# Kernel tuning notes

Measured on AMD Instinct MI355X. Metric: run time of the kernel, lower is better.

Reference implementation:

```python
import jax, jax.numpy as jnp
import numpy as np

N_WIDTH = 16
N_ORDER = 3
N_ELEMENTS = 64
N_NODES = N_ELEMENTS * N_ORDER + 1  # 193
N_SAMPLES = 4096
X_MIN = 0.0
X_MAX = 1.0
NDIM_IN = 2


def setup_inputs() -> dict:
    key = jax.random.key(0)
    k1, k2 = jax.random.split(key)
    x = jax.random.uniform(k1, (N_SAMPLES, NDIM_IN), dtype=jnp.float32)  # in [x_min, x_max]
    # torch init is zeros; use small random values so outputs/grads are informative
    weight = 0.1 * jax.random.normal(k2, (N_WIDTH, N_NODES, NDIM_IN), dtype=jnp.float32)
    return {"x": x, "weight": weight}


def _lagrange_all(xr, nodes):
    """phi, dphi, ddphi of the (n_order+1) Lagrange basis at xr (S,W,D).
    Returns three arrays of shape (S,W,P,D), P = n_order+1. Loops are over the
    tiny fixed basis size only; everything is vectorized over (S,W,D)."""
    P = len(nodes)
    phi, dphi, ddphi = [], [], []
    for j in range(P):
        # value
        p = jnp.ones_like(xr)
        for m in range(P):
            if m != j:
                p = p * (xr - nodes[m]) / (nodes[j] - nodes[m])
        phi.append(p)
        # first derivative
        y1 = jnp.zeros_like(xr)
        for i in range(P):
            if i == j:
                continue
            k = jnp.full_like(xr, 1.0 / (nodes[j] - nodes[i]))
            for m in range(P):
                if m != i and m != j:
                    k = k * (xr - nodes[m]) / (nodes[j] - nodes[m])
            y1 = y1 + k
        dphi.append(y1)
        # second derivative
        y2 = jnp.zeros_like(xr)
        for i in range(P):
            if i == j:
                continue
            ks = jnp.zeros_like(xr)
            for m in range(P):
                if m != i and m != j:
                    kp = jnp.full_like(xr, 1.0 / (nodes[j] - nodes[m]))
                    for n in range(P):
                        if n != i and n != j and n != m:
                            kp = kp * (xr - nodes[n]) / (nodes[j] - nodes[n])
                    ks = ks + kp
            y2 = y2 + ks / (nodes[j] - nodes[i])
        ddphi.append(y2)
    return jnp.stack(phi, 2), jnp.stack(dphi, 2), jnp.stack(ddphi, 2)


def _forward(x, weight):
    S, W, D, P = N_SAMPLES, N_WIDTH, NDIM_IN, N_ORDER + 1
    xw = jnp.broadcast_to(x[:, None, :], (S, W, D))  # (S,W,D)
    x_shift = (N_NODES - 1) * (xw - X_MIN) / (X_MAX - X_MIN)
    id_el = jnp.clip(jnp.floor(x_shift / N_ORDER), 0, N_ELEMENTS - 1)
    nodes_l = (id_el * N_ORDER).astype(jnp.int32)  # (S,W,D), left node index
    # nodes_r - nodes_l == n_order
    x_ref = 2.0 * (x_shift - nodes_l) / N_ORDER - 1.0
    delta_x = 0.5 * N_ORDER * (X_MAX - X_MIN) / (N_NODES - 1)

    nodes = [float(v) for v in np.linspace(-1.0, 1.0, P)]
    phi_l, dphi_l, ddphi_l = _lagrange_all(x_ref, nodes)  # (S,W,P,D)
    dphi_l = dphi_l / delta_x
    ddphi_l = ddphi_l / (delta_x * delta_x)

    # Scatter local basis values into global node axis (vectorized replacement
    # of the quadruple Python loop in the original).
    ii = jnp.arange(S)[:, None, None, None]
    kk = jnp.arange(W)[None, :, None, None]
    dd = jnp.arange(D)[None, None, None, :]
    pp = nodes_l[:, :, None, :] + jnp.arange(P)[None, None, :, None]  # (S,W,P,D)
    zeros = jnp.zeros((S, W, N_NODES, D), dtype=x.dtype)
    phi = zeros.at[ii, kk, pp, dd].set(phi_l)
    dphi = zeros.at[ii, kk, pp, dd].set(dphi_l)
    ddphi = zeros.at[ii, kk, pp, dd].set(ddphi_l)

    t_ik = jnp.einsum('kpj,ikpj->ik', weight, phi)
    dt_ik = jnp.einsum('kpj,ikpj->ik', weight, dphi)
    ddt_ik = jnp.einsum('kpj,ikpj->ik', weight, ddphi)
    return t_ik, dt_ik, ddt_ik, phi, dphi, ddphi, delta_x


def reference(x, weight):
    # returns (t_ik, dt_ik, ddt_ik, phi_ikpj, dphi_ikpj, ddphi_ikpj, delta_x)
    return _forward(x, weight)
```

## Files before the change

### kernel.cpp

```cpp
#include <hip/hip_runtime.h>

constexpr int S  = 4096;
constexpr int W  = 16;
constexpr int NN = 193;
constexpr int DD = 2;
constexpr int SW = S * W;
constexpr int PHI_OFF = 3 * SW;
constexpr int PHI_SZ  = SW * NN * DD;
constexpr int DX_OFF  = PHI_OFF + 3 * PHI_SZ;

constexpr int ROW_F  = NN * DD;
constexpr int ROW_F2 = NN;
constexpr int CHUNK_F2 = W * ROW_F2;

__global__ __launch_bounds__(256)
void kan_fused_kernel(const float* __restrict__ x,
                      const float* __restrict__ w,
                      float* __restrict__ out) {
    const int i   = blockIdx.x;
    const int tid = threadIdx.x;

    __shared__ __align__(16) float row[3][ROW_F];
    __shared__ float vals[3][DD][4];
    __shared__ int   nls[DD];

    for (int idx = tid; idx < 3 * ROW_F; idx += 256)
        (&row[0][0])[idx] = 0.0f;

    if (tid < DD) {
        const int d = tid;
        float xv = x[i * DD + d];
        float xs = 192.0f * xv;
        float fe = floorf(xs / 3.0f);
        fe = fminf(fmaxf(fe, 0.0f), 63.0f);
        int nl = (int)(fe * 3.0f);
        nls[d] = nl;
        float xr = 2.0f * (xs - (float)nl) / 3.0f - 1.0f;

        float xp1 = xr + 1.0f;
        float xm1 = xr - 1.0f;
        float x2  = xr * xr;
        float x2m = x2 - (1.0f / 9.0f);
        const float c0 = 0.5625f;
        const float c1 = 1.6875f;

        vals[0][d][0] = -c0 * x2m * xm1;
        vals[0][d][1] =  c1 * xp1 * (xr - (1.0f / 3.0f)) * xm1;
        vals[0][d][2] = -c1 * xp1 * (xr + (1.0f / 3.0f)) * xm1;
        vals[0][d][3] =  c0 * xp1 * x2m;

        const float idx1 = 128.0f;
        vals[1][d][0] = -c0 * (3.0f * x2 - 2.0f * xr - (1.0f / 9.0f)) * idx1;
        vals[1][d][1] =  c1 * (3.0f * x2 - (2.0f / 3.0f) * xr - 1.0f) * idx1;
        vals[1][d][2] = -c1 * (3.0f * x2 + (2.0f / 3.0f) * xr - 1.0f) * idx1;
        vals[1][d][3] =  c0 * (3.0f * x2 + 2.0f * xr - (1.0f / 9.0f)) * idx1;

        const float idx2 = 16384.0f;
        vals[2][d][0] = -c0 * (6.0f * xr - 2.0f) * idx2;
        vals[2][d][1] =  c1 * (6.0f * xr - (2.0f / 3.0f)) * idx2;
        vals[2][d][2] = -c1 * (6.0f * xr + (2.0f / 3.0f)) * idx2;
        vals[2][d][3] =  c0 * (6.0f * xr + 2.0f) * idx2;
    }

    __syncthreads();

    if (tid < 24) {
        int a = tid >> 3;
        int r = tid & 7;
        int d = r >> 2;
        int p = r & 3;
        row[a][(nls[d] + p) * DD + d] = vals[a][d][p];
    }

    if (tid < 48) {
        int k = tid / 3;
        int a = tid % 3;
        float s = 0.0f;
#pragma unroll
        for (int d = 0; d < DD; ++d) {
            int base = k * (NN * DD) + nls[d] * DD + d;
#pragma unroll
            for (int p = 0; p < 4; ++p)
                s += w[base + p * DD] * vals[a][d][p];
        }
        out[a * SW + i * W + k] = s;
    }

    if (i == 0 && tid == 0)
        out[DX_OFF] = 0.0078125f;

    __syncthreads();

#pragma unroll
    for (int a = 0; a < 3; ++a) {
        float2* dst = (float2*)(out + PHI_OFF + a * PHI_SZ) + (size_t)i * CHUNK_F2;
        const float2* src = (const float2*)(&row[a][0]);
        for (int idx = tid; idx < CHUNK_F2; idx += 256) {
            int j = idx % ROW_F2;
            dst[idx] = src[j];
        }
    }
}

extern "C" void kernel_launch(void* const* d_in, const int* in_sizes, int n_in,
                              void* d_out, int out_size, void* d_ws, size_t ws_size,
                              hipStream_t stream) {
    const float* x = (const float*)d_in[0];
    const float* w = (const float*)d_in[1];
    float* out = (float*)d_out;

    kan_fused_kernel<<<S, 256, 0, stream>>>(x, w, out);
}
```

Measured before the change: 302.6 us.

## Process eight samples per block with 16-byte nontemporal stores of phi rows

Each block now handles 8 samples instead of 1 and builds padded shared-memory rows for all of them. The phi, dphi and ddphi output is written as 16-byte vectors with nontemporal stores instead of 8-byte float2 stores. Row wrap-around is handled by padding each row so a 4-float read can cross the row end. This is meant to raise store width and cut per-block overhead on a kernel limited by output writes, at the cost of fewer blocks and more shared memory per block.

```diff
diff --git a/kernel.cpp b/kernel.cpp
--- a/kernel.cpp
+++ b/kernel.cpp
@@ -9,32 +9,44 @@
 constexpr int PHI_SZ  = SW * NN * DD;
 constexpr int DX_OFF  = PHI_OFF + 3 * PHI_SZ;
 
-constexpr int ROW_F  = NN * DD;
-constexpr int ROW_F2 = NN;
-constexpr int CHUNK_F2 = W * ROW_F2;
+constexpr int ROW_F   = NN * DD;
+constexpr int ROW_PAD = 392;
+constexpr int R       = 8;
+constexpr int NB      = S / R;
+constexpr int CHUNK_F = W * ROW_F;
+constexpr int BLK_F4  = R * CHUNK_F / 4;
+constexpr int FULL_IT = BLK_F4 / 256;
+constexpr int TAIL    = BLK_F4 - FULL_IT * 256;
+constexpr int STEP_J  = 1024 % ROW_F;
+
+typedef float f32x4 __attribute__((ext_vector_type(4)));
 
 __global__ __launch_bounds__(256)
 void kan_fused_kernel(const float* __restrict__ x,
                       const float* __restrict__ w,
                       float* __restrict__ out) {
-    const int i   = blockIdx.x;
+    const int bx  = blockIdx.x;
     const int tid = threadIdx.x;
 
-    __shared__ __align__(16) float row[3][ROW_F];
-    __shared__ float vals[3][DD][4];
-    __shared__ int   nls[DD];
+    __shared__ __align__(16) float row[3][R][ROW_PAD];
+    __shared__ float vals[3][R][DD][4];
+    __shared__ int   nls[R][DD];
 
-    for (int idx = tid; idx < 3 * ROW_F; idx += 256)
-        (&row[0][0])[idx] = 0.0f;
+    {
+        f32x4* rz = (f32x4*)&row[0][0][0];
+        for (int idx = tid; idx < 3 * R * ROW_PAD / 4; idx += 256)
+            rz[idx] = (f32x4){0.f, 0.f, 0.f, 0.f};
+    }
 
-    if (tid < DD) {
-        const int d = tid;
-        float xv = x[i * DD + d];
+    if (tid < R * DD) {
+        const int smp = tid >> 1;
+        const int d   = tid & 1;
+        float xv = x[(bx * R + smp) * DD + d];
         float xs = 192.0f * xv;
         float fe = floorf(xs / 3.0f);
         fe = fminf(fmaxf(fe, 0.0f), 63.0f);
         int nl = (int)(fe * 3.0f);
-        nls[d] = nl;
+        nls[smp][d] = nl;
         float xr = 2.0f * (xs - (float)nl) / 3.0f - 1.0f;
 
         float xp1 = xr + 1.0f;
@@ -44,60 +56,92 @@
         const float c0 = 0.5625f;
         const float c1 = 1.6875f;
 
-        vals[0][d][0] = -c0 * x2m * xm1;
-        vals[0][d][1] =  c1 * xp1 * (xr - (1.0f / 3.0f)) * xm1;
-        vals[0][d][2] = -c1 * xp1 * (xr + (1.0f / 3.0f)) * xm1;
-        vals[0][d][3] =  c0 * xp1 * x2m;
+        vals[0][smp][d][0] = -c0 * x2m * xm1;
+        vals[0][smp][d][1] =  c1 * xp1 * (xr - (1.0f / 3.0f)) * xm1;
+        vals[0][smp][d][2] = -c1 * xp1 * (xr + (1.0f / 3.0f)) * xm1;
+        vals[0][smp][d][3] =  c0 * xp1 * x2m;
 
         const float idx1 = 128.0f;
-        vals[1][d][0] = -c0 * (3.0f * x2 - 2.0f * xr - (1.0f / 9.0f)) * idx1;
-        vals[1][d][1] =  c1 * (3.0f * x2 - (2.0f / 3.0f) * xr - 1.0f) * idx1;
-        vals[1][d][2] = -c1 * (3.0f * x2 + (2.0f / 3.0f) * xr - 1.0f) * idx1;
-        vals[1][d][3] =  c0 * (3.0f * x2 + 2.0f * xr - (1.0f / 9.0f)) * idx1;
+        vals[1][smp][d][0] = -c0 * (3.0f * x2 - 2.0f * xr - (1.0f / 9.0f)) * idx1;
+        vals[1][smp][d][1] =  c1 * (3.0f * x2 - (2.0f / 3.0f) * xr - 1.0f) * idx1;
+        vals[1][smp][d][2] = -c1 * (3.0f * x2 + (2.0f / 3.0f) * xr - 1.0f) * idx1;
+        vals[1][smp][d][3] =  c0 * (3.0f * x2 + 2.0f * xr - (1.0f / 9.0f)) * idx1;
 
         const float idx2 = 16384.0f;
-        vals[2][d][0] = -c0 * (6.0f * xr - 2.0f) * idx2;
-        vals[2][d][1] =  c1 * (6.0f * xr - (2.0f / 3.0f)) * idx2;
-        vals[2][d][2] = -c1 * (6.0f * xr + (2.0f / 3.0f)) * idx2;
-        vals[2][d][3] =  c0 * (6.0f * xr + 2.0f) * idx2;
+        vals[2][smp][d][0] = -c0 * (6.0f * xr - 2.0f) * idx2;
+        vals[2][smp][d][1] =  c1 * (6.0f * xr - (2.0f / 3.0f)) * idx2;
+        vals[2][smp][d][2] = -c1 * (6.0f * xr + (2.0f / 3.0f)) * idx2;
+        vals[2][smp][d][3] =  c0 * (6.0f * xr + 2.0f) * idx2;
     }
 
     __syncthreads();
 
-    if (tid < 24) {
-        int a = tid >> 3;
-        int r = tid & 7;
-        int d = r >> 2;
-        int p = r & 3;
-        row[a][(nls[d] + p) * DD + d] = vals[a][d][p];
+    if (tid < 192) {
+        int a = tid >> 6;
+        int r = tid & 63;
+        int smp = r >> 3;
+        int rr  = r & 7;
+        int d = rr >> 2;
+        int p = rr & 3;
+        row[a][smp][(nls[smp][d] + p) * DD + d] = vals[a][smp][d][p];
+    } else if (tid < 240) {
+        int q = tid - 192;
+        int a = q >> 4;
+        int r = q & 15;
+        int smp = r >> 1;
+        int d   = r & 1;
+        if (nls[smp][d] == 0)
+            row[a][smp][ROW_F + d] = vals[a][smp][d][0];
     }
 
-    if (tid < 48) {
-        int k = tid / 3;
-        int a = tid % 3;
+    for (int t = tid; t < R * W * 3; t += 256) {
+        int smp = t / 48;
+        int r2  = t % 48;
+        int k = r2 / 3;
+        int a = r2 % 3;
         float s = 0.0f;
 #pragma unroll
         for (int d = 0; d < DD; ++d) {
-            int base = k * (NN * DD) + nls[d] * DD + d;
+            int base = k * ROW_F + nls[smp][d] * DD + d;
 #pragma unroll
             for (int p = 0; p < 4; ++p)
-                s += w[base + p * DD] * vals[a][d][p];
+                s += w[base + p * DD] * vals[a][smp][d][p];
         }
-        out[a * SW + i * W + k] = s;
+        out[a * SW + (bx * R + smp) * W + k] = s;
     }
 
-    if (i == 0 && tid == 0)
+    if (bx == 0 && tid == 0)
         out[DX_OFF] = 0.0078125f;
 
     __syncthreads();
 
+    int j0 = tid * 4;
+    if (j0 >= ROW_F) j0 -= ROW_F;
+    if (j0 >= ROW_F) j0 -= ROW_F;
+
 #pragma unroll
     for (int a = 0; a < 3; ++a) {
-        float2* dst = (float2*)(out + PHI_OFF + a * PHI_SZ) + (size_t)i * CHUNK_F2;
-        const float2* src = (const float2*)(&row[a][0]);
-        for (int idx = tid; idx < CHUNK_F2; idx += 256) {
-            int j = idx % ROW_F2;
-            dst[idx] = src[j];
+        f32x4* dst = (f32x4*)(out + PHI_OFF + (size_t)a * PHI_SZ
+                                  + (size_t)bx * (R * CHUNK_F));
+        const float* rowa = &row[a][0][0];
+        int j = j0, fs = tid * 4, smp = 0, nn = tid;
+#pragma unroll 4
+        for (int it = 0; it < FULL_IT; ++it) {
+            const float* rp = rowa + smp * ROW_PAD;
+            float2 u = *(const float2*)&rp[j];
+            float2 v = *(const float2*)&rp[j + 2];
+            __builtin_nontemporal_store((f32x4){u.x, u.y, v.x, v.y}, &dst[nn]);
+            nn += 256;
+            fs += 1024;
+            if (fs >= CHUNK_F) { fs -= CHUNK_F; smp += 1; }
+            j += STEP_J;
+            if (j >= ROW_F) j -= ROW_F;
+        }
+        if (tid < TAIL) {
+            const float* rp = rowa + smp * ROW_PAD;
+            float2 u = *(const float2*)&rp[j];
+            float2 v = *(const float2*)&rp[j + 2];
+            __builtin_nontemporal_store((f32x4){u.x, u.y, v.x, v.y}, &dst[nn]);
         }
     }
 }
@@ -109,5 +153,5 @@
     const float* w = (const float*)d_in[1];
     float* out = (float*)d_out;
 
-    kan_fused_kernel<<<S, 256, 0, stream>>>(x, w, out);
+    kan_fused_kernel<<<NB, 256, 0, stream>>>(x, w, out);
 }
```

Measured after the change: 313.5 us. 3.6% more time.

## Split into per-sample basis pass and grid-stride vectorized phi fill pass

Applied to the files above, without the earlier changes.

Replaces the one-block-per-sample fused kernel with two kernels. The first computes the basis values and the weighted sums one thread per sample, storing compact basis values and node indices in workspace. The second is a flat grid-stride kernel that writes the huge sparse phi/dphi/ddphi tensors with 16-byte stores, computing each element from the compact workspace. The aim is fully coalesced, evenly distributed streaming writes of the dominant output, at the cost of a second launch and extra index arithmetic.

```diff
diff --git a/kernel.cpp b/kernel.cpp
--- a/kernel.cpp
+++ b/kernel.cpp
@@ -7,35 +7,43 @@
 constexpr int SW = S * W;
 constexpr int PHI_OFF = 3 * SW;
 constexpr int PHI_SZ  = SW * NN * DD;
-constexpr int DX_OFF  = PHI_OFF + 3 * PHI_SZ;
+constexpr long long DX_OFF = (long long)PHI_OFF + 3LL * PHI_SZ;
 
-constexpr int ROW_F  = NN * DD;
-constexpr int ROW_F2 = NN;
-constexpr int CHUNK_F2 = W * ROW_F2;
+constexpr int ROW_F    = NN * DD;
+constexpr int CHUNK_F4 = ROW_F * W / 4;
+constexpr long long G4TOT = 3LL * PHI_SZ / 4;
+
+constexpr int P2B     = 2048;
+constexpr int TPB     = 256;
+constexpr int STRIDE4 = P2B * TPB;
+constexpr int DQ = STRIDE4 % CHUNK_F4;
+constexpr int DI = STRIDE4 / CHUNK_F4;
+constexpr int DM = (4 * DQ) % ROW_F;
+
+constexpr int VWS_FLOATS = 3 * DD * 4 * S;
+constexpr size_t NWS_OFF = (size_t)VWS_FLOATS * 4;
+
+typedef float f32x4 __attribute__((ext_vector_type(4)));
 
 __global__ __launch_bounds__(256)
-void kan_fused_kernel(const float* __restrict__ x,
-                      const float* __restrict__ w,
-                      float* __restrict__ out) {
-    const int i   = blockIdx.x;
-    const int tid = threadIdx.x;
+void kan_pass1(const float* __restrict__ x, const float* __restrict__ w,
+               float* __restrict__ out, float* __restrict__ vws,
+               unsigned* __restrict__ nws) {
+    const int i = blockIdx.x * 256 + threadIdx.x;
+    if (i >= S) return;
 
-    __shared__ __align__(16) float row[3][ROW_F];
-    __shared__ float vals[3][DD][4];
-    __shared__ int   nls[DD];
+    float v[3][DD][4];
+    int   nl[DD];
 
-    for (int idx = tid; idx < 3 * ROW_F; idx += 256)
-        (&row[0][0])[idx] = 0.0f;
-
-    if (tid < DD) {
-        const int d = tid;
+#pragma unroll
+    for (int d = 0; d < DD; ++d) {
         float xv = x[i * DD + d];
         float xs = 192.0f * xv;
         float fe = floorf(xs / 3.0f);
         fe = fminf(fmaxf(fe, 0.0f), 63.0f);
-        int nl = (int)(fe * 3.0f);
-        nls[d] = nl;
-        float xr = 2.0f * (xs - (float)nl) / 3.0f - 1.0f;
+        int n = (int)(fe * 3.0f);
+        nl[d] = n;
+        float xr = 2.0f * (xs - (float)n) / 3.0f - 1.0f;
 
         float xp1 = xr + 1.0f;
         float xm1 = xr - 1.0f;
@@ -44,61 +52,99 @@
         const float c0 = 0.5625f;
         const float c1 = 1.6875f;
 
-        vals[0][d][0] = -c0 * x2m * xm1;
-        vals[0][d][1] =  c1 * xp1 * (xr - (1.0f / 3.0f)) * xm1;
-        vals[0][d][2] = -c1 * xp1 * (xr + (1.0f / 3.0f)) * xm1;
-        vals[0][d][3] =  c0 * xp1 * x2m;
+        v[0][d][0] = -c0 * x2m * xm1;
+        v[0][d][1] =  c1 * xp1 * (xr - (1.0f / 3.0f)) * xm1;
+        v[0][d][2] = -c1 * xp1 * (xr + (1.0f / 3.0f)) * xm1;
+        v[0][d][3] =  c0 * xp1 * x2m;
 
         const float idx1 = 128.0f;
-        vals[1][d][0] = -c0 * (3.0f * x2 - 2.0f * xr - (1.0f / 9.0f)) * idx1;
-        vals[1][d][1] =  c1 * (3.0f * x2 - (2.0f / 3.0f) * xr - 1.0f) * idx1;
-        vals[1][d][2] = -c1 * (3.0f * x2 + (2.0f / 3.0f) * xr - 1.0f) * idx1;
-        vals[1][d][3] =  c0 * (3.0f * x2 + 2.0f * xr - (1.0f / 9.0f)) * idx1;
+        v[1][d][0] = -c0 * (3.0f * x2 - 2.0f * xr - (1.0f / 9.0f)) * idx1;
+        v[1][d][1] =  c1 * (3.0f * x2 - (2.0f / 3.0f) * xr - 1.0f) * idx1;
+        v[1][d][2] = -c1 * (3.0f * x2 + (2.0f / 3.0f) * xr - 1.0f) * idx1;
+        v[1][d][3] =  c0 * (3.0f * x2 + 2.0f * xr - (1.0f / 9.0f)) * idx1;
 
         const float idx2 = 16384.0f;
-        vals[2][d][0] = -c0 * (6.0f * xr - 2.0f) * idx2;
-        vals[2][d][1] =  c1 * (6.0f * xr - (2.0f / 3.0f)) * idx2;
-        vals[2][d][2] = -c1 * (6.0f * xr + (2.0f / 3.0f)) * idx2;
-        vals[2][d][3] =  c0 * (6.0f * xr + 2.0f) * idx2;
+        v[2][d][0] = -c0 * (6.0f * xr - 2.0f) * idx2;
+        v[2][d][1] =  c1 * (6.0f * xr - (2.0f / 3.0f)) * idx2;
+        v[2][d][2] = -c1 * (6.0f * xr + (2.0f / 3.0f)) * idx2;
+        v[2][d][3] =  c0 * (6.0f * xr + 2.0f) * idx2;
     }
 
-    __syncthreads();
+    nws[i] = (unsigned)nl[0] | ((unsigned)nl[1] << 8);
 
-    if (tid < 24) {
-        int a = tid >> 3;
-        int r = tid & 7;
-        int d = r >> 2;
-        int p = r & 3;
-        row[a][(nls[d] + p) * DD + d] = vals[a][d][p];
-    }
-
-    if (tid < 48) {
-        int k = tid / 3;
-        int a = tid % 3;
-        float s = 0.0f;
 #pragma unroll
-        for (int d = 0; d < DD; ++d) {
-            int base = k * (NN * DD) + nls[d] * DD + d;
+    for (int a = 0; a < 3; ++a)
+#pragma unroll
+        for (int d = 0; d < DD; ++d)
 #pragma unroll
             for (int p = 0; p < 4; ++p)
-                s += w[base + p * DD] * vals[a][d][p];
-        }
-        out[a * SW + i * W + k] = s;
-    }
-
-    if (i == 0 && tid == 0)
-        out[DX_OFF] = 0.0078125f;
-
-    __syncthreads();
+                vws[((a * 2 + d) * 4 + p) * S + i] = v[a][d][p];
 
 #pragma unroll
     for (int a = 0; a < 3; ++a) {
-        float2* dst = (float2*)(out + PHI_OFF + a * PHI_SZ) + (size_t)i * CHUNK_F2;
-        const float2* src = (const float2*)(&row[a][0]);
-        for (int idx = tid; idx < CHUNK_F2; idx += 256) {
-            int j = idx % ROW_F2;
-            dst[idx] = src[j];
+        float s[W];
+#pragma unroll
+        for (int k = 0; k < W; ++k) {
+            float acc = 0.0f;
+#pragma unroll
+            for (int d = 0; d < DD; ++d) {
+                int base = k * ROW_F + nl[d] * DD + d;
+#pragma unroll
+                for (int p = 0; p < 4; ++p)
+                    acc += w[base + p * DD] * v[a][d][p];
+            }
+            s[k] = acc;
         }
+        f32x4* o4 = (f32x4*)(out + (size_t)a * SW + (size_t)i * W);
+#pragma unroll
+        for (int q = 0; q < 4; ++q)
+            o4[q] = (f32x4){s[4 * q], s[4 * q + 1], s[4 * q + 2], s[4 * q + 3]};
+    }
+
+    if (i == 0)
+        out[DX_OFF] = 0.0078125f;
+}
+
+__global__ __launch_bounds__(256)
+void kan_pass2(float* __restrict__ out, const float* __restrict__ vws,
+               const unsigned* __restrict__ nws) {
+    const int g0 = blockIdx.x * 256 + threadIdx.x;
+
+    unsigned I = (unsigned)g0 / CHUNK_F4;
+    unsigned q = (unsigned)g0 - I * CHUNK_F4;
+    unsigned m = (q * 4u) % ROW_F;
+
+    f32x4* p4 = (f32x4*)(out + PHI_OFF) + g0;
+
+    for (long long g = g0; g < G4TOT; g += STRIDE4) {
+        const unsigned i  = I & (unsigned)(S - 1);
+        const unsigned a  = I >> 12;
+        const unsigned pk = nws[i];
+        const int n0 = (int)(m >> 1);
+        const int n1 = (m == (unsigned)(ROW_F - 2)) ? 0 : n0 + 1;
+        const int nl0 = (int)(pk & 0xFFu);
+        const int nl1 = (int)(pk >> 8);
+
+        const unsigned ux = (unsigned)(n0 - nl0);
+        const unsigned uy = (unsigned)(n0 - nl1);
+        const unsigned uz = (unsigned)(n1 - nl0);
+        const unsigned uw = (unsigned)(n1 - nl1);
+
+        f32x4 v = (f32x4){0.f, 0.f, 0.f, 0.f};
+        if ((ux < 4u) | (uy < 4u) | (uz < 4u) | (uw < 4u)) {
+            const float* vb = vws + (size_t)a * (8 * S) + i;
+            if (ux < 4u) v.x = vb[(0 * 4 + (int)ux) * S];
+            if (uy < 4u) v.y = vb[(1 * 4 + (int)uy) * S];
+            if (uz < 4u) v.z = vb[(0 * 4 + (int)uz) * S];
+            if (uw < 4u) v.w = vb[(1 * 4 + (int)uw) * S];
+        }
+        *p4 = v;
+
+        p4 += STRIDE4;
+        q += DQ; I += DI;
+        if (q >= (unsigned)CHUNK_F4) { q -= CHUNK_F4; ++I; }
+        m += DM;
+        if (m >= (unsigned)ROW_F) m -= ROW_F;
     }
 }
 
@@ -109,5 +155,9 @@
     const float* w = (const float*)d_in[1];
     float* out = (float*)d_out;
 
-    kan_fused_kernel<<<S, 256, 0, stream>>>(x, w, out);
+    float*    vws = (float*)d_ws;
+    unsigned* nws = (unsigned*)((char*)d_ws + NWS_OFF);
+
+    kan_pass1<<<(S + 255) / 256, 256, 0, stream>>>(x, w, out, vws, nws);
+    kan_pass2<<<P2B, TPB, 0, stream>>>(out, vws, nws);
 }
```

Result: slower. 327.2 us (+8.1%).
